# Kernel optimization log

Measured on AMD Instinct MI355X. Metric: run time of the kernel, lower is better.

Reference implementation:

```python
import jax, jax.numpy as jnp
import numpy as np

N = 10000      # nodes
E = 100000     # edges
C = 32         # in_channels == hidden_channels == out_channels
ED = 4         # edge_dim
G = 64         # number of graphs in the batch
EPS = 1e-5     # BatchNorm eps


def setup_inputs() -> dict:
    key = jax.random.key(0)
    ks = jax.random.split(key, 20)
    rn = lambda k, shape, s=0.05: jax.random.normal(k, shape, dtype=jnp.float32) * s
    return {
        "x": jax.random.normal(ks[0], (N, C), dtype=jnp.float32),
        "edge_attr": jax.random.normal(ks[1], (E, ED), dtype=jnp.float32),
        # edge MLP 1: ED -> C -> C*C ; NNConv1 root/bias
        "e1_w1": rn(ks[2], (ED, C)), "e1_b1": jnp.zeros((C,), jnp.float32),
        "e1_w2": rn(ks[3], (C, C * C)), "e1_b2": jnp.zeros((C * C,), jnp.float32),
        "root1": rn(ks[4], (C, C)), "bias1": jnp.zeros((C,), jnp.float32),
        # edge MLP 2: ED -> C -> C*C ; NNConv2 root/bias
        "e2_w1": rn(ks[5], (ED, C)), "e2_b1": jnp.zeros((C,), jnp.float32),
        "e2_w2": rn(ks[6], (C, C * C)), "e2_b2": jnp.zeros((C * C,), jnp.float32),
        "root2": rn(ks[7], (C, C)), "bias2": jnp.zeros((C,), jnp.float32),
        # BatchNorm (eval mode: running stats)
        "bn1_g": jnp.ones((C,), jnp.float32), "bn1_b": jnp.zeros((C,), jnp.float32),
        "bn1_m": rn(ks[8], (C,), 0.1), "bn1_v": 1.0 + 0.1 * jax.random.uniform(ks[9], (C,), dtype=jnp.float32),
        "bn2_g": jnp.ones((C,), jnp.float32), "bn2_b": jnp.zeros((C,), jnp.float32),
        "bn2_m": rn(ks[10], (C,), 0.1), "bn2_v": 1.0 + 0.1 * jax.random.uniform(ks[11], (C,), dtype=jnp.float32),
        # readout: C -> C//2 -> 1
        "r1_w": rn(ks[12], (C, C // 2)), "r1_b": jnp.zeros((C // 2,), jnp.float32),
        "r2_w": rn(ks[13], (C // 2, 1)), "r2_b": jnp.zeros((1,), jnp.float32),
        "edge_index": jax.random.randint(ks[14], (2, E), 0, N),
        "batch": jnp.sort(jax.random.randint(ks[15], (N,), 0, G)),
    }


def _nnconv(x, edge_index, edge_attr, w1, b1, w2, b2, root, bias):
    # edge MLP -> per-edge weight matrix [E, C, C]
    h = jax.nn.relu(edge_attr @ w1 + b1)
    W = (h @ w2 + b2).reshape(E, C, C)
    src, dst = edge_index[0], edge_index[1]
    # gather source features, per-edge matmul, scatter-mean to target nodes
    msg = jnp.einsum('ei,eio->eo', x[src], W)                      # [E, C]
    agg = jax.ops.segment_sum(msg, dst, num_segments=N)            # [N, C]
    cnt = jax.ops.segment_sum(jnp.ones((E,), x.dtype), dst, num_segments=N)
    agg = agg / jnp.maximum(cnt, 1.0)[:, None]
    return agg + x @ root + bias


def _bn(x, g, b, m, v):
    return (x - m) * jax.lax.rsqrt(v + EPS) * g + b


def reference(x, edge_attr,
              e1_w1, e1_b1, e1_w2, e1_b2, root1, bias1,
              e2_w1, e2_b1, e2_w2, e2_b2, root2, bias2,
              bn1_g, bn1_b, bn1_m, bn1_v,
              bn2_g, bn2_b, bn2_m, bn2_v,
              r1_w, r1_b, r2_w, r2_b,
              edge_index, batch):
    h = jax.nn.relu(_bn(_nnconv(x, edge_index, edge_attr, e1_w1, e1_b1, e1_w2, e1_b2, root1, bias1),
                        bn1_g, bn1_b, bn1_m, bn1_v))
    h = jax.nn.relu(_bn(_nnconv(h, edge_index, edge_attr, e2_w1, e2_b1, e2_w2, e2_b2, root2, bias2),
                        bn2_g, bn2_b, bn2_m, bn2_v))
    # global mean pool over graphs
    psum = jax.ops.segment_sum(h, batch, num_segments=G)           # [G, C]
    pcnt = jax.ops.segment_sum(jnp.ones((N,), h.dtype), batch, num_segments=G)
    pooled = psum / jnp.maximum(pcnt, 1.0)[:, None]
    # readout MLP (dropout is identity in eval)
    return jax.nn.relu(pooled @ r1_w + r1_b) @ r2_w + r2_b          # [G, 1]
```

## Files before the change

kernel.cpp:

```cpp
#include <hip/hip_runtime.h>

#define NN 10000
#define EE 100000
#define CC 32
#define GG 64
#define EPSV 1e-5f
#define NB 8
#define SLOTS 1056
#define HST 32
#define PST 36
#define PNODE (32*PST)
#define CAP 126
#define HBLK ((EE+255)/256)
#define WBLK 160

__global__ __launch_bounds__(256) void k_pre(const int* __restrict__ ei,
        int* __restrict__ cnt, int* __restrict__ deg,
        const float* __restrict__ w2a, const float* __restrict__ b2a,
        const float* __restrict__ w2b, const float* __restrict__ b2b,
        float* __restrict__ w2r1, float* __restrict__ w2r2) {
    int blk = blockIdx.x;
    int t = threadIdx.x;
    if (blk < HBLK) {
        int e = blk * 256 + t;
        if (e < EE) {
            atomicAdd(&cnt[ei[EE + e]], 1);
            atomicAdd(&deg[ei[e]], 1);
        }
    } else {
        int b2i = blk - HBLK;
        int s = (b2i % 5) * 256 + t;
        int i = b2i / 5;
        if (s < SLOTS) {
            float va = (s < 1024) ? w2a[(s >> 5) * 1024 + i * 32 + (s & 31)]
                                  : b2a[i * 32 + (s - 1024)];
            float vb = (s < 1024) ? w2b[(s >> 5) * 1024 + i * 32 + (s & 31)]
                                  : b2b[i * 32 + (s - 1024)];
            w2r1[i * SLOTS + s] = va;
            w2r2[i * SLOTS + s] = vb;
        }
    }
}

__global__ __launch_bounds__(1024) void k_scan(const int* __restrict__ deg,
                                               const int* __restrict__ cnt,
                                               int* __restrict__ rowptr,
                                               int* __restrict__ cursor,
                                               int* __restrict__ colptr,
                                               int* __restrict__ ccursor) {
    __shared__ int buf[1024];
    int t = threadIdx.x;
    int base = t * 10;
    for (int pass = 0; pass < 2; pass++) {
        const int* src = pass ? cnt : deg;
        int* dst_p = pass ? colptr : rowptr;
        int* dst_c = pass ? ccursor : cursor;
        int v[10]; int s = 0;
        #pragma unroll
        for (int k = 0; k < 10; k++) {
            int idx = base + k;
            v[k] = (idx < NN) ? src[idx] : 0;
            s += v[k];
        }
        buf[t] = s;
        for (int off = 1; off < 1024; off <<= 1) {
            __syncthreads();
            int val = buf[t] + ((t >= off) ? buf[t - off] : 0);
            __syncthreads();
            buf[t] = val;
        }
        __syncthreads();
        int carry = (t > 0) ? buf[t - 1] : 0;
        #pragma unroll
        for (int k = 0; k < 10; k++) {
            int idx = base + k;
            if (idx < NN) { dst_p[idx] = carry; dst_c[idx] = carry; }
            carry += v[k];
        }
        if (t == 1023) dst_p[NN] = buf[1023];
        __syncthreads();
    }
}

__global__ __launch_bounds__(256) void k_scatter(const int* __restrict__ ei,
        const float* __restrict__ edge_attr,
        const float* __restrict__ w1a, const float* __restrict__ b1a,
        const float* __restrict__ w1b, const float* __restrict__ b1b,
        int* __restrict__ cursor, int* __restrict__ ccursor,
        int* __restrict__ msrc, int* __restrict__ cpos,
        float* __restrict__ hbuf1, float* __restrict__ hbuf2) {
    __shared__ float wsh[320];
    int t = threadIdx.x;
    for (int s = t; s < 320; s += 256) {
        wsh[s] = (s < 128) ? w1a[s]
               : (s < 160) ? b1a[s - 128]
               : (s < 288) ? w1b[s - 160]
                           : b1b[s - 288];
    }
    __syncthreads();
    int e = blockIdx.x * 256 + t;
    if (e >= EE) return;
    int sn = ei[e];
    int dn = ei[EE + e];
    float4 a = *(const float4*)&edge_attr[(size_t)e * 4];
    int pos = atomicAdd(&cursor[sn], 1);
    msrc[pos] = sn;
    int cp = atomicAdd(&ccursor[dn], 1);
    cpos[cp] = pos;
    float h1v[32], h2v[32];
    #pragma unroll
    for (int o = 0; o < 32; o++) {
        h1v[o] = fmaxf(a.x * wsh[o]       + a.y * wsh[32 + o]  + a.z * wsh[64 + o]  + a.w * wsh[96 + o]  + wsh[128 + o], 0.f);
        h2v[o] = fmaxf(a.x * wsh[160 + o] + a.y * wsh[192 + o] + a.z * wsh[224 + o] + a.w * wsh[256 + o] + wsh[288 + o], 0.f);
    }
    #pragma unroll
    for (int ob = 0; ob < 8; ob++) {
        *(float4*)&hbuf1[(size_t)pos * HST + 4 * ob] =
            make_float4(h1v[4 * ob], h1v[4 * ob + 1], h1v[4 * ob + 2], h1v[4 * ob + 3]);
        *(float4*)&hbuf2[(size_t)pos * HST + 4 * ob] =
            make_float4(h2v[4 * ob], h2v[4 * ob + 1], h2v[4 * ob + 2], h2v[4 * ob + 3]);
    }
}

__global__ __launch_bounds__(256, 3) void k_fused3(const float* __restrict__ x,
        const float* __restrict__ hbuf,
        const float* __restrict__ w2r,
        const int* __restrict__ msrc, const int* __restrict__ rowptr,
        float* __restrict__ msg) {
    __shared__ float xs[NB][32];
    __shared__ float P2[NB * PNODE];
    __shared__ float sh_h[CAP * HST];
    __shared__ int   sh_src[CAP];
    int t = threadIdx.x;
    int o = t & 31;
    int cb = 4 * (t >> 5);
    int n0 = blockIdx.x * NB;

    int ebase = rowptr[n0];
    int eend  = rowptr[n0 + NB];
    int ne    = eend - ebase;
    int ne_st = (ne < CAP) ? ne : CAP;

    const float4* hsrc4 = (const float4*)&hbuf[(size_t)ebase * HST];
    int nvec = ne_st * (HST / 4);
    float4 rv[4];
    #pragma unroll
    for (int k = 0; k < 4; k++) {
        int vi = t + 256 * k;
        if (vi < nvec) rv[k] = hsrc4[vi];
    }
    int msv = n0;
    if (t < ne_st) msv = msrc[ebase + t];

    xs[t >> 5][t & 31] = x[n0 * 32 + t];
    __syncthreads();

    {
        float acc[4][NB];
        #pragma unroll
        for (int k = 0; k < 4; k++)
            #pragma unroll
            for (int n = 0; n < NB; n++) acc[k][n] = 0.f;
        #pragma unroll
        for (int j = 0; j < 8; j++) {
            float wk[4][4];
            #pragma unroll
            for (int r = 0; r < 4; r++)
                #pragma unroll
                for (int k = 0; k < 4; k++)
                    wk[r][k] = w2r[(4 * j + r) * SLOTS + (cb + k) * 32 + o];
            #pragma unroll
            for (int n = 0; n < NB; n++) {
                float4 xq = *(const float4*)&xs[n][4 * j];
                #pragma unroll
                for (int k = 0; k < 4; k++)
                    acc[k][n] += xq.x * wk[0][k] + xq.y * wk[1][k]
                               + xq.z * wk[2][k] + xq.w * wk[3][k];
            }
        }
        #pragma unroll
        for (int n = 0; n < NB; n++) {
            float4 st = make_float4(acc[0][n], acc[1][n], acc[2][n], acc[3][n]);
            *(float4*)&P2[n * PNODE + o * PST + cb] = st;
        }
    }
    if (t < 32) {
        float wb[32];
        #pragma unroll
        for (int i = 0; i < 32; i++) wb[i] = w2r[i * SLOTS + 1024 + t];
        #pragma unroll
        for (int n = 0; n < NB; n++) {
            float b = 0.f;
            #pragma unroll
            for (int j = 0; j < 8; j++) {
                float4 xq = *(const float4*)&xs[n][4 * j];
                b += xq.x * wb[4 * j] + xq.y * wb[4 * j + 1]
                   + xq.z * wb[4 * j + 2] + xq.w * wb[4 * j + 3];
            }
            *(float4*)&P2[n * PNODE + t * PST + 32] = make_float4(b, 0.f, 0.f, 0.f);
        }
    }

    {
        float4* hdst = (float4*)sh_h;
        #pragma unroll
        for (int k = 0; k < 4; k++) {
            int vi = t + 256 * k;
            if (vi < nvec) hdst[vi] = rv[k];
        }
        if (t < ne_st) sh_src[t] = msv;
    }
    __syncthreads();

    int grp = t >> 5;
    int idx = grp;
    int src_c = n0;
    if (idx < ne) src_c = (idx < ne_st) ? sh_src[idx] : msrc[ebase + idx];
    while (idx < ne) {
        int idx_n = idx + 8;
        int src_n = src_c;
        if (idx_n < ne) src_n = (idx_n < ne_st) ? sh_src[idx_n] : msrc[ebase + idx_n];
        const float* Pn = &P2[(src_c - n0) * PNODE + o * PST];
        float m = Pn[32];
        if (idx < ne_st) {
            const float* hr = &sh_h[idx * HST];
            #pragma unroll
            for (int b = 0; b < 8; b++) {
                float4 hqv = *(const float4*)&hr[4 * b];
                float4 pq  = *(const float4*)&Pn[4 * b];
                m += hqv.x * pq.x + hqv.y * pq.y + hqv.z * pq.z + hqv.w * pq.w;
            }
        } else {
            const float* hr = &hbuf[(size_t)(ebase + idx) * HST];
            #pragma unroll
            for (int b = 0; b < 8; b++) {
                float4 hqv = *(const float4*)&hr[4 * b];
                float4 pq  = *(const float4*)&Pn[4 * b];
                m += hqv.x * pq.x + hqv.y * pq.y + hqv.z * pq.z + hqv.w * pq.w;
            }
        }
        msg[(size_t)(ebase + idx) * 32 + o] = m;
        idx = idx_n; src_c = src_n;
    }
}

__global__ __launch_bounds__(256) void k_combine(const float* __restrict__ x_in,
        const float* __restrict__ msg,
        const int* __restrict__ colptr, const int* __restrict__ cpos,
        const float* __restrict__ root, const float* __restrict__ bias,
        const float* __restrict__ bng, const float* __restrict__ bnb,
        const float* __restrict__ bnm, const float* __restrict__ bnv,
        float* __restrict__ x_out, float* __restrict__ psum,
        const int* __restrict__ batch) {
    __shared__ float xs[8][32];
    __shared__ float vals[8][32];
    __shared__ int gb[8];
    int t = threadIdx.x;
    int n0 = blockIdx.x * 8;
    xs[t >> 5][t & 31] = x_in[n0 * 32 + t];
    __syncthreads();
    int k = t >> 5, o = t & 31, n = n0 + k;
    float r = bias[o];
    #pragma unroll
    for (int i = 0; i < 32; i++) r += xs[k][i] * root[i * 32 + o];
    int jbase = colptr[n], jend = colptr[n + 1];
    float acc = 0.f;
    for (int jb = jbase; jb < jend; jb += 32) {
        int nrem = jend - jb;
        int lim = (nrem < 32) ? nrem : 32;
        int cv = 0;
        if (o < lim) cv = cpos[jb + o];
        for (int j = 0; j < lim; j += 8) {
            float v[8];
            #pragma unroll
            for (int q = 0; q < 8; q++) {
                if (j + q < lim) {
                    int cj = __shfl(cv, j + q, 32);
                    v[q] = msg[(size_t)cj * 32 + o];
                } else v[q] = 0.f;
            }
            #pragma unroll
            for (int q = 0; q < 8; q++) acc += v[q];
        }
    }
    float a = acc / fmaxf((float)(jend - jbase), 1.f);
    float val = a + r;
    val = (val - bnm[o]) * rsqrtf(bnv[o] + EPSV) * bng[o] + bnb[o];
    val = fmaxf(val, 0.f);
    if (x_out) {
        x_out[(size_t)n * 32 + o] = val;
    }
    if (psum) {
        vals[k][o] = val;
        if (o == 0) gb[k] = batch[n];
        __syncthreads();
        if (k == 0) {
            float pacc = vals[0][o];
            int g = gb[0];
            #pragma unroll
            for (int k2 = 1; k2 < 8; k2++) {
                if (gb[k2] == g) pacc += vals[k2][o];
                else {
                    atomicAdd(&psum[(size_t)g * 32 + o], pacc);
                    g = gb[k2]; pacc = vals[k2][o];
                }
            }
            atomicAdd(&psum[(size_t)g * 32 + o], pacc);
        }
    }
}

__global__ __launch_bounds__(256) void k_readout(const float* __restrict__ psum,
        const int* __restrict__ batch,
        const float* __restrict__ r1w, const float* __restrict__ r1b,
        const float* __restrict__ r2w, const float* __restrict__ r2b,
        float* __restrict__ out) {
    __shared__ float w1s[32 * 16];
    __shared__ float b1s[16];
    __shared__ float w2s[16];
    __shared__ float ps[GG * 32];
    int t = threadIdx.x;
    int cnt_g = 0;
    if (t < GG) {
        int lo = 0, hi = NN;
        while (lo < hi) { int m = (lo + hi) >> 1; if (batch[m] < t) lo = m + 1; else hi = m; }
        int lb = lo;
        lo = 0; hi = NN;
        while (lo < hi) { int m = (lo + hi) >> 1; if (batch[m] < t + 1) lo = m + 1; else hi = m; }
        cnt_g = lo - lb;
    }
    w1s[t] = r1w[t];
    w1s[t + 256] = r1w[t + 256];
    if (t < 16) { b1s[t] = r1b[t]; w2s[t] = r2w[t]; }
    #pragma unroll
    for (int i = 0; i < GG * 32 / 256; i++) ps[t + i * 256] = psum[t + i * 256];
    __syncthreads();
    if (t < GG) {
        float inv = 1.f / fmaxf((float)cnt_g, 1.f);
        float acc = r2b[0];
        #pragma unroll
        for (int j = 0; j < 16; j++) {
            float dot = 0.f;
            #pragma unroll
            for (int c = 0; c < 32; c++) dot += ps[t * 32 + c] * w1s[c * 16 + j];
            float z = dot * inv + b1s[j];
            acc += fmaxf(z, 0.f) * w2s[j];
        }
        out[t] = acc;
    }
}

extern "C" void kernel_launch(void* const* d_in, const int* in_sizes, int n_in,
                              void* d_out, int out_size, void* d_ws, size_t ws_size,
                              hipStream_t stream) {
    const float* x       = (const float*)d_in[0];
    const float* eattr   = (const float*)d_in[1];
    const float* e1_w1   = (const float*)d_in[2];
    const float* e1_b1   = (const float*)d_in[3];
    const float* e1_w2   = (const float*)d_in[4];
    const float* e1_b2   = (const float*)d_in[5];
    const float* root1   = (const float*)d_in[6];
    const float* bias1   = (const float*)d_in[7];
    const float* e2_w1   = (const float*)d_in[8];
    const float* e2_b1   = (const float*)d_in[9];
    const float* e2_w2   = (const float*)d_in[10];
    const float* e2_b2   = (const float*)d_in[11];
    const float* root2   = (const float*)d_in[12];
    const float* bias2   = (const float*)d_in[13];
    const float* bn1_g   = (const float*)d_in[14];
    const float* bn1_b   = (const float*)d_in[15];
    const float* bn1_m   = (const float*)d_in[16];
    const float* bn1_v   = (const float*)d_in[17];
    const float* bn2_g   = (const float*)d_in[18];
    const float* bn2_b   = (const float*)d_in[19];
    const float* bn2_m   = (const float*)d_in[20];
    const float* bn2_v   = (const float*)d_in[21];
    const float* r1_w    = (const float*)d_in[22];
    const float* r1_b    = (const float*)d_in[23];
    const float* r2_w    = (const float*)d_in[24];
    const float* r2_b    = (const float*)d_in[25];
    const int*   ei      = (const int*)d_in[26];
    const int*   batch   = (const int*)d_in[27];

    char* ws = (char*)d_ws;
    float* hbuf1  = (float*)(ws);
    float* hbuf2  = (float*)(ws + 12800000);
    float* w2r1   = (float*)(ws + 25600000);
    float* w2r2   = (float*)(ws + 25735168);
    float* msg    = (float*)(ws + 25870336);
    int*   cnt    = (int*)  (ws + 38670336);
    int*   deg    = (int*)  (ws + 38710336);
    float* psum   = (float*)(ws + 38750336);
    float* xmid   = (float*)(ws + 38758528);
    int*   rowptr = (int*)  (ws + 40038528);
    int*   cursor = (int*)  (ws + 40078592);
    int*   colptr = (int*)  (ws + 40118592);
    int*   ccursor= (int*)  (ws + 40158656);
    int*   msrc   = (int*)  (ws + 40198656);
    int*   cpos   = (int*)  (ws + 40598656);

    hipMemsetAsync(ws + 38670336, 0, 88192, stream);

    k_pre<<<HBLK + WBLK, 256, 0, stream>>>(ei, cnt, deg,
                                           e1_w2, e1_b2, e2_w2, e2_b2, w2r1, w2r2);
    k_scan<<<1, 1024, 0, stream>>>(deg, cnt, rowptr, cursor, colptr, ccursor);
    k_scatter<<<(EE + 255) / 256, 256, 0, stream>>>(ei, eattr,
                                                    e1_w1, e1_b1, e2_w1, e2_b1,
                                                    cursor, ccursor, msrc, cpos,
                                                    hbuf1, hbuf2);

    k_fused3<<<NN / NB, 256, 0, stream>>>(x, hbuf1, w2r1, msrc, rowptr, msg);
    k_combine<<<NN / 8, 256, 0, stream>>>(x, msg, colptr, cpos, root1, bias1,
                                          bn1_g, bn1_b, bn1_m, bn1_v,
                                          xmid, nullptr, batch);

    k_fused3<<<NN / NB, 256, 0, stream>>>(xmid, hbuf2, w2r2, msrc, rowptr, msg);
    k_combine<<<NN / 8, 256, 0, stream>>>(xmid, msg, colptr, cpos, root2, bias2,
                                          bn2_g, bn2_b, bn2_m, bn2_v,
                                          nullptr, psum, batch);

    k_readout<<<1, 256, 0, stream>>>(psum, batch, r1_w, r1_b, r2_w, r2_b, (float*)d_out);
}
```

Before: 287.7 us.

## Replace LDS staging of edge hidden rows with register double-buffered prefetch

Removes the shared-memory staging of per-edge hidden vectors and source indices in k_fused3. Each warp group instead double-buffers two edges' hidden rows in registers, prefetching the edge 16 positions ahead while computing the current one. This frees LDS, so occupancy is raised to 4 blocks per SM, and the global-memory latency is overlapped with the P2 dot products. The cost is higher register pressure from 64 float4 registers, which may cause spills under the tighter launch bound.

```diff
diff --git a/kernel.cpp b/kernel.cpp
--- a/kernel.cpp
+++ b/kernel.cpp
@@ -10,7 +10,6 @@
 #define HST 32
 #define PST 36
 #define PNODE (32*PST)
-#define CAP 126
 #define HBLK ((EE+255)/256)
 #define WBLK 160
 
@@ -122,15 +121,13 @@
     }
 }
 
-__global__ __launch_bounds__(256, 3) void k_fused3(const float* __restrict__ x,
+__global__ __launch_bounds__(256, 4) void k_fused3(const float* __restrict__ x,
         const float* __restrict__ hbuf,
         const float* __restrict__ w2r,
         const int* __restrict__ msrc, const int* __restrict__ rowptr,
         float* __restrict__ msg) {
     __shared__ float xs[NB][32];
     __shared__ float P2[NB * PNODE];
-    __shared__ float sh_h[CAP * HST];
-    __shared__ int   sh_src[CAP];
     int t = threadIdx.x;
     int o = t & 31;
     int cb = 4 * (t >> 5);
@@ -138,19 +135,6 @@
 
     int ebase = rowptr[n0];
     int eend  = rowptr[n0 + NB];
-    int ne    = eend - ebase;
-    int ne_st = (ne < CAP) ? ne : CAP;
-
-    const float4* hsrc4 = (const float4*)&hbuf[(size_t)ebase * HST];
-    int nvec = ne_st * (HST / 4);
-    float4 rv[4];
-    #pragma unroll
-    for (int k = 0; k < 4; k++) {
-        int vi = t + 256 * k;
-        if (vi < nvec) rv[k] = hsrc4[vi];
-    }
-    int msv = n0;
-    if (t < ne_st) msv = msrc[ebase + t];
 
     xs[t >> 5][t & 31] = x[n0 * 32 + t];
     __syncthreads();
@@ -200,47 +184,64 @@
             *(float4*)&P2[n * PNODE + t * PST + 32] = make_float4(b, 0.f, 0.f, 0.f);
         }
     }
-
-    {
-        float4* hdst = (float4*)sh_h;
-        #pragma unroll
-        for (int k = 0; k < 4; k++) {
-            int vi = t + 256 * k;
-            if (vi < nvec) hdst[vi] = rv[k];
-        }
-        if (t < ne_st) sh_src[t] = msv;
-    }
     __syncthreads();
 
     int grp = t >> 5;
-    int idx = grp;
-    int src_c = n0;
-    if (idx < ne) src_c = (idx < ne_st) ? sh_src[idx] : msrc[ebase + idx];
-    while (idx < ne) {
-        int idx_n = idx + 8;
-        int src_n = src_c;
-        if (idx_n < ne) src_n = (idx_n < ne_st) ? sh_src[idx_n] : msrc[ebase + idx_n];
-        const float* Pn = &P2[(src_c - n0) * PNODE + o * PST];
-        float m = Pn[32];
-        if (idx < ne_st) {
-            const float* hr = &sh_h[idx * HST];
+    int pos = ebase + grp;
+
+    int srcA = n0, srcB = n0;
+    float4 hqA[8], hqB[8];
+    if (pos < eend) {
+        srcA = msrc[pos];
+        const float* h0 = &hbuf[(size_t)pos * HST];
+        #pragma unroll
+        for (int b = 0; b < 8; b++) hqA[b] = *(const float4*)&h0[4 * b];
+    }
+    if (pos + 8 < eend) {
+        srcB = msrc[pos + 8];
+        const float* h1 = &hbuf[(size_t)(pos + 8) * HST];
+        #pragma unroll
+        for (int b = 0; b < 8; b++) hqB[b] = *(const float4*)&h1[4 * b];
+    }
+
+    while (pos < eend) {
+        {
+            const float* Pn = &P2[(srcA - n0) * PNODE + o * PST];
+            float m = Pn[32];
             #pragma unroll
             for (int b = 0; b < 8; b++) {
-                float4 hqv = *(const float4*)&hr[4 * b];
-                float4 pq  = *(const float4*)&Pn[4 * b];
-                m += hqv.x * pq.x + hqv.y * pq.y + hqv.z * pq.z + hqv.w * pq.w;
-            }
-        } else {
-            const float* hr = &hbuf[(size_t)(ebase + idx) * HST];
+                float4 pq = *(const float4*)&Pn[4 * b];
+                m += hqA[b].x * pq.x + hqA[b].y * pq.y + hqA[b].z * pq.z + hqA[b].w * pq.w;
+            }
+            msg[(size_t)pos * 32 + o] = m;
+            int p2 = pos + 16;
+            if (p2 < eend) {
+                srcA = msrc[p2];
+                const float* hn = &hbuf[(size_t)p2 * HST];
+                #pragma unroll
+                for (int b = 0; b < 8; b++) hqA[b] = *(const float4*)&hn[4 * b];
+            }
+        }
+        pos += 8;
+        if (pos >= eend) break;
+        {
+            const float* Pn = &P2[(srcB - n0) * PNODE + o * PST];
+            float m = Pn[32];
             #pragma unroll
             for (int b = 0; b < 8; b++) {
-                float4 hqv = *(const float4*)&hr[4 * b];
-                float4 pq  = *(const float4*)&Pn[4 * b];
-                m += hqv.x * pq.x + hqv.y * pq.y + hqv.z * pq.z + hqv.w * pq.w;
-            }
-        }
-        msg[(size_t)(ebase + idx) * 32 + o] = m;
-        idx = idx_n; src_c = src_n;
+                float4 pq = *(const float4*)&Pn[4 * b];
+                m += hqB[b].x * pq.x + hqB[b].y * pq.y + hqB[b].z * pq.z + hqB[b].w * pq.w;
+            }
+            msg[(size_t)pos * 32 + o] = m;
+            int p3 = pos + 16;
+            if (p3 < eend) {
+                srcB = msrc[p3];
+                const float* hn = &hbuf[(size_t)p3 * HST];
+                #pragma unroll
+                for (int b = 0; b < 8; b++) hqB[b] = *(const float4*)&hn[4 * b];
+            }
+        }
+        pos += 8;
     }
 }
 
```

New measurement: 427.4 us. +48.5%, slower.
